# Performance work log

Hardware: AMD Instinct MI355X
Metric: run time of the kernel (lower is better)

The kernel has to match this reference:

```python
import jax, jax.numpy as jnp
import numpy as np

B, S, D = 2, 2048, 2048
H, KVH, HD = 16, 4, 128
ROT = 64  # partial rotary dims (cos/sin last dim = ROT//2)
WINDOW = 1024
EPS = 1e-6


def _rmsnorm(x, scale=None):
    x32 = x.astype(jnp.float32)
    y = x32 * jax.lax.rsqrt(jnp.mean(x32 * x32, axis=-1, keepdims=True) + EPS)
    if scale is not None:
        y = y * (1.0 + scale.astype(jnp.float32))
    return y.astype(x.dtype)


def _rope(x, cos, sin):
    # x: [b, h, s, hd]; rotate first ROT dims, pass through the rest
    x_rot, x_pass = x[..., :ROT], x[..., ROT:]
    x1, x2 = x_rot[..., :ROT // 2], x_rot[..., ROT // 2:]
    rotated = jnp.concatenate([-x2, x1], axis=-1)
    cos_f = jnp.concatenate([cos, cos], axis=-1)[None, None].astype(x.dtype)
    sin_f = jnp.concatenate([sin, sin], axis=-1)[None, None].astype(x.dtype)
    return jnp.concatenate([x_rot * cos_f + rotated * sin_f, x_pass], axis=-1)


def setup_inputs() -> dict:
    key = jax.random.key(0)
    ks = jax.random.split(key, 6)
    x = jax.random.normal(ks[0], (B, S, D), jnp.float32)
    # causal + sliding-window mask (True = masked out)
    i = jnp.arange(S)
    rel = i[:, None] - i[None, :]  # query - key
    mask = (rel < 0) | (rel >= WINDOW)
    # RoPE tables
    inv_freq = 1.0 / (10000.0 ** (jnp.arange(0, ROT, 2, dtype=jnp.float32) / ROT))
    t = jnp.arange(S, dtype=jnp.float32)[:, None] * inv_freq[None, :]  # [S, ROT//2]
    cos, sin = jnp.cos(t), jnp.sin(t)
    init = 0.02
    Wq = jax.random.normal(ks[1], (D, H * HD), jnp.float32) * init
    Wk = jax.random.normal(ks[2], (D, KVH * HD), jnp.float32) * init
    Wv = jax.random.normal(ks[3], (D, KVH * HD), jnp.float32) * init
    Wo = jax.random.normal(ks[4], (H * HD, D), jnp.float32) * init
    q_scale = jnp.zeros((HD,), jnp.float32)  # Gemma RMSNorm weight init = 0, applied as (1+w)
    k_scale = jnp.zeros((HD,), jnp.float32)
    return {"x": x, "mask": mask, "cos": cos, "sin": sin,
            "Wq": Wq, "Wk": Wk, "Wv": Wv, "Wo": Wo,
            "q_scale": q_scale, "k_scale": k_scale}


def reference(x, mask, cos, sin, Wq, Wk, Wv, Wo, q_scale, k_scale):
    b, s, _ = x.shape
    G = H // KVH  # group size
    q = (x @ Wq).reshape(b, s, H, HD).transpose(0, 2, 1, 3)      # [b,H,s,hd]
    q = _rope(_rmsnorm(q, q_scale), cos, sin)
    k = (x @ Wk).reshape(b, s, KVH, HD).transpose(0, 2, 1, 3)    # [b,KVH,s,hd]
    k = _rope(_rmsnorm(k, k_scale), cos, sin)
    v = _rmsnorm((x @ Wv).reshape(b, s, KVH, HD).transpose(0, 2, 1, 3))
    # grouped-head attention (equivalent to repeat_interleave of k/v over groups)
    qg = q.reshape(b, KVH, G, s, HD)
    scores = jnp.einsum('bkgqd,bkld->bkgql', qg, k)              # no 1/sqrt(hd): QK-norm model
    scores = jnp.where(mask[None, None, None], -jnp.inf, scores)
    w = jax.nn.softmax(scores.astype(jnp.float32), axis=-1).astype(q.dtype)
    ctx = jnp.einsum('bkgql,bkld->bkgqd', w, v)                  # [b,KVH,G,s,hd]
    ctx = ctx.reshape(b, H, s, HD).transpose(0, 2, 1, 3).reshape(b, s, H * HD)
    return ctx @ Wo
```

## Files before the change

### kernel.cpp

```cpp
#include <hip/hip_runtime.h>
#include <stdint.h>

#define B_ 2
#define S_ 2048
#define D_ 2048
#define H_ 16
#define KVH_ 4
#define HD_ 128
#define ROT_ 64
#define WINDOW_ 1024
#define EPS_ 1e-6f
#define M_ (B_ * S_)
#define NQKV_ 3072

#define QBLK 128
#define KVBLK 64
#define LOG2E 1.44269504088896340736f
#define DEFER_THR 8.0f

typedef unsigned short ushort_t;
typedef _Float16 f16;
typedef float f32x4 __attribute__((ext_vector_type(4)));
typedef f16 f16x8 __attribute__((ext_vector_type(8)));

#define NINF (-__builtin_inff())
#define EXP2F(x) __builtin_exp2f(x)

__device__ __forceinline__ void gload16(const void* g, void* l) {
  __builtin_amdgcn_global_load_lds(
      (const __attribute__((address_space(1))) void*)g,
      (__attribute__((address_space(3))) void*)l, 16, 0, 0);
}

__launch_bounds__(256, 4)
__global__ void cast_f32_f16(const float* __restrict__ src, f16* __restrict__ dst, int n8) {
  int i = blockIdx.x * 256 + threadIdx.x;
  if (i >= n8) return;
  float4 a = reinterpret_cast<const float4*>(src)[i * 2];
  float4 b = reinterpret_cast<const float4*>(src)[i * 2 + 1];
  f16x8 o = { (f16)a.x, (f16)a.y, (f16)a.z, (f16)a.w,
              (f16)b.x, (f16)b.y, (f16)b.z, (f16)b.w };
  reinterpret_cast<f16x8*>(dst)[i] = o;
}

__launch_bounds__(256, 4)
__global__ void transpose_f32_f16(const float* __restrict__ src, f16* __restrict__ dst,
                                  int R, int C) {
  __shared__ float tile[32][33];
  int c0 = blockIdx.x * 32, r0 = blockIdx.y * 32;
  int tx = threadIdx.x & 31, ty = threadIdx.x >> 5;
#pragma unroll
  for (int i = 0; i < 32; i += 8)
    tile[ty + i][tx] = src[(size_t)(r0 + ty + i) * C + c0 + tx];
  __syncthreads();
#pragma unroll
  for (int i = 0; i < 32; i += 8)
    dst[(size_t)(c0 + ty + i) * R + r0 + tx] = (f16)tile[tx][ty + i];
}

__launch_bounds__(256, 4)
__global__ void transpose16(const ushort_t* __restrict__ src, ushort_t* __restrict__ dst,
                            int R, int C) {
  __shared__ ushort_t tile[32][33];
  size_t base = (size_t)blockIdx.z * R * C;
  src += base; dst += base;
  int c0 = blockIdx.x * 32, r0 = blockIdx.y * 32;
  int tx = threadIdx.x & 31, ty = threadIdx.x >> 5;
#pragma unroll
  for (int i = 0; i < 32; i += 8)
    tile[ty + i][tx] = src[(size_t)(r0 + ty + i) * C + c0 + tx];
  __syncthreads();
#pragma unroll
  for (int i = 0; i < 32; i += 8)
    dst[(size_t)(c0 + ty + i) * R + r0 + tx] = tile[tx][ty + i];
}

__launch_bounds__(256, 2)
__global__ void gemm_f16(const f16* __restrict__ A, const f16* __restrict__ Bt,
                         float* __restrict__ C, int M, int N, int K) {
  __shared__ __attribute__((aligned(16))) f16 As[128][64];
  __shared__ __attribute__((aligned(16))) f16 Bs[128][64];
  const int gx = gridDim.x;
  const int nwg = gx * gridDim.y;
  const int flat = blockIdx.y * gx + blockIdx.x;
  const int q8 = nwg >> 3;
  const int id2 = (flat & 7) * q8 + (flat >> 3);
  const int bm = (id2 / gx) * 128, bn = (id2 % gx) * 128;
  const int tid = threadIdx.x;
  const int lane = tid & 63, wid = tid >> 6;
  const int wm = (wid >> 1) * 64, wn = (wid & 1) * 64;
  const int rr = lane & 15, rg = lane >> 4;
  const int sw = (((lane & 7) ^ (lane >> 3)) << 4);
  const int srw = lane >> 3;
  const char* Ab = (const char*)A + ((size_t)(bm + wid * 32 + srw) * K) * 2 + sw;
  const char* Bb = (const char*)Bt + ((size_t)(bn + wid * 32 + srw) * K) * 2 + sw;
  f32x4 acc[4][4] = {};
  for (int k0 = 0; k0 < K; k0 += 64) {
    __syncthreads();
#pragma unroll
    for (int g = 0; g < 4; ++g) {
      gload16(Ab + (size_t)(g * 8) * K * 2 + (size_t)k0 * 2,
              (char*)&As[0][0] + (wid * 32 + g * 8) * 128);
      gload16(Bb + (size_t)(g * 8) * K * 2 + (size_t)k0 * 2,
              (char*)&Bs[0][0] + (wid * 32 + g * 8) * 128);
    }
    __syncthreads();
    f16x8 af[4][2], bf[4][2];
#pragma unroll
    for (int i = 0; i < 4; ++i)
#pragma unroll
      for (int kk = 0; kk < 2; ++kk) {
        af[i][kk] = *reinterpret_cast<const f16x8*>(
            (const char*)&As[0][0] + (wm + i * 16 + rr) * 128 +
            ((kk * 64 + rg * 16) ^ ((rr & 7) << 4)));
        bf[i][kk] = *reinterpret_cast<const f16x8*>(
            (const char*)&Bs[0][0] + (wn + i * 16 + rr) * 128 +
            ((kk * 64 + rg * 16) ^ ((rr & 7) << 4)));
      }
#pragma unroll
    for (int kk = 0; kk < 2; ++kk)
#pragma unroll
      for (int i = 0; i < 4; ++i)
#pragma unroll
        for (int j = 0; j < 4; ++j)
          acc[i][j] = __builtin_amdgcn_mfma_f32_16x16x32_f16(af[i][kk], bf[j][kk],
                                                             acc[i][j], 0, 0, 0);
  }
#pragma unroll
  for (int i = 0; i < 4; ++i)
#pragma unroll
    for (int j = 0; j < 4; ++j)
#pragma unroll
      for (int r = 0; r < 4; ++r)
        C[(size_t)(bm + wm + i * 16 + rg * 4 + r) * N + (bn + wn + j * 16 + rr)] = acc[i][j][r];
}

__launch_bounds__(256, 4)
__global__ void norm_rope_kv(const float* __restrict__ qkv, const float* __restrict__ cosb,
                             const float* __restrict__ sinb, const float* __restrict__ ksc,
                             f16* __restrict__ kf, f16* __restrict__ vb) {
  int gw = blockIdx.x * 4 + (threadIdx.x >> 6);
  int lane = threadIdx.x & 63;
  int row = gw >> 3, c = gw & 7;
  int b = row >> 11, s = row & (S_ - 1);
  int col = (c < 4) ? (2048 + c * 128) : (2560 + (c - 4) * 128);
  const float* src = qkv + (size_t)row * NQKV_ + col;
  float2 v = *reinterpret_cast<const float2*>(src + lane * 2);
  float ss = v.x * v.x + v.y * v.y;
#pragma unroll
  for (int off = 32; off; off >>= 1) ss += __shfl_xor(ss, off);
  float inv = rsqrtf(ss * (1.0f / HD_) + EPS_);
  float x0 = v.x * inv, x1 = v.y * inv;
  int d0 = lane * 2;
  f16* dst;
  size_t idx;
  if (c < 4) {
    x0 *= (1.0f + ksc[d0]);
    x1 *= (1.0f + ksc[d0 + 1]);
    float y0 = __shfl_xor(x0, 16);
    float y1 = __shfl_xor(x1, 16);
    if (d0 < ROT_) {
      int dm = d0 & 31;
      float cs0 = cosb[s * 32 + dm],     sn0 = sinb[s * 32 + dm];
      float cs1 = cosb[s * 32 + dm + 1], sn1 = sinb[s * 32 + dm + 1];
      if (d0 < 32) { x0 = x0 * cs0 - y0 * sn0; x1 = x1 * cs1 - y1 * sn1; }
      else         { x0 = x0 * cs0 + y0 * sn0; x1 = x1 * cs1 + y1 * sn1; }
    }
    x0 *= LOG2E; x1 *= LOG2E;
    dst = kf; idx = ((size_t)((b * KVH_ + c) * S_ + s)) * HD_ + d0;
  } else {
    dst = vb; idx = ((size_t)((b * KVH_ + (c - 4)) * S_ + s)) * HD_ + d0;
  }
  f16 o[2] = { (f16)x0, (f16)x1 };
  unsigned int pk; __builtin_memcpy(&pk, o, 4);
  *reinterpret_cast<unsigned int*>(dst + idx) = pk;
}

__launch_bounds__(256, 2)
__global__ void flash_attn(const float* __restrict__ qkv, const float* __restrict__ cosb,
                           const float* __restrict__ sinb, const float* __restrict__ qsc,
                           const f16* __restrict__ kfp, const f16* __restrict__ vt,
                           f16* __restrict__ ctxf) {
  __shared__ __attribute__((aligned(16))) f16 Ks[2][KVBLK][128];
  __shared__ __attribute__((aligned(16))) f16 Vs[2][128][KVBLK];
  __shared__ __attribute__((aligned(16))) f16 Pb[4][32][40];
  const int id = blockIdx.x;
  const int g8 = id & 7, rest = id >> 3;
  const int b = g8 >> 2, kvh = g8 & 3;
  int hh, qtile;
  if (rest < 32) { hh = rest >> 3; qtile = 8 + (rest & 7); }
  else { int lv = rest - 32; hh = lv >> 3; qtile = lv & 7; }
  const int h = kvh * 4 + hh;
  const int lane = threadIdx.x & 63, w = threadIdx.x >> 6;
  const int rr = lane & 15, rg = lane >> 4;
  const int qBase = qtile * QBLK;
  const int qw = qBase + w * 32;
  const f16* Kh = kfp + (size_t)(b * KVH_ + kvh) * S_ * HD_;
  const f16* Vh = vt  + (size_t)(b * KVH_ + kvh) * HD_ * S_;

  f16x8 qf[2][4];
#pragma unroll
  for (int rb = 0; rb < 2; ++rb) {
    const int srow = qw + rb * 16 + rr;
    const float* qrow = qkv + (size_t)(b * S_ + srow) * NQKV_ + h * HD_;
    float qv[4][8];
    float ssq = 0.f;
#pragma unroll
    for (int kk = 0; kk < 4; ++kk) {
      float4 u0 = *reinterpret_cast<const float4*>(qrow + kk * 32 + rg * 8);
      float4 u1 = *reinterpret_cast<const float4*>(qrow + kk * 32 + rg * 8 + 4);
      qv[kk][0] = u0.x; qv[kk][1] = u0.y; qv[kk][2] = u0.z; qv[kk][3] = u0.w;
      qv[kk][4] = u1.x; qv[kk][5] = u1.y; qv[kk][6] = u1.z; qv[kk][7] = u1.w;
#pragma unroll
      for (int j = 0; j < 8; ++j) ssq += qv[kk][j] * qv[kk][j];
    }
    ssq += __shfl_xor(ssq, 16);
    ssq += __shfl_xor(ssq, 32);
    float inv = rsqrtf(ssq * (1.0f / HD_) + EPS_);
#pragma unroll
    for (int kk = 0; kk < 4; ++kk)
#pragma unroll
      for (int j = 0; j < 8; ++j)
        qv[kk][j] *= inv * (1.0f + qsc[kk * 32 + rg * 8 + j]);
    const float* cs = cosb + (size_t)srow * 32;
    const float* sn = sinb + (size_t)srow * 32;
#pragma unroll
    for (int j = 0; j < 8; ++j) {
      int d = rg * 8 + j;
      float c = cs[d], s = sn[d];
      float x0 = qv[0][j], x1 = qv[1][j];
      qv[0][j] = x0 * c - x1 * s;
      qv[1][j] = x1 * c + x0 * s;
    }
#pragma unroll
    for (int kk = 0; kk < 4; ++kk)
#pragma unroll
      for (int j = 0; j < 8; ++j)
        qf[rb][kk][j] = (f16)qv[kk][j];
  }

  f32x4 acc[2][8] = {};
  f32x4 accl[2] = {};
  float m_run[2][4], msafe[2][4];
#pragma unroll
  for (int rb = 0; rb < 2; ++rb)
#pragma unroll
    for (int r = 0; r < 4; ++r) { m_run[rb][r] = NINF; msafe[rb][r] = 0.f; }
  const f16x8 ones = { (f16)1, (f16)1, (f16)1, (f16)1, (f16)1, (f16)1, (f16)1, (f16)1 };

  int kvStart = qBase - (WINDOW_ - 1);
  if (kvStart < 0) kvStart = 0;
  kvStart &= ~(KVBLK - 1);
  const int ntile = (qBase + QBLK - kvStart) >> 6;

  const int k_r0 = lane >> 4;
  const int k_cb = (lane & 15) * 16;
  const int v_r0 = lane >> 3;
  const int v_cb = (lane & 7) * 16;

#define STAGE(bufs, key0_)                                                           \
  do {                                                                               \
    _Pragma("unroll")                                                                \
    for (int gg = 0; gg < 4; ++gg) {                                                 \
      int krow = gg * 4 + k_r0;                                                      \
      gload16((const char*)Kh + (size_t)((key0_) + w * 16 + krow) * 256 +            \
                  (k_cb ^ ((krow & 7) << 4)),                                        \
              (char*)&Ks[bufs][0][0] + (w * 16 + gg * 4) * 256);                     \
      int vrow = gg * 8 + v_r0;                                                      \
      gload16((const char*)Vh + (size_t)(w * 32 + vrow) * (S_ * 2) +                 \
                  (size_t)(key0_) * 2 + (v_cb ^ ((vrow & 7) << 4)),                  \
              (char*)&Vs[bufs][0][0] + (w * 32 + gg * 8) * 128);                     \
    }                                                                                \
  } while (0)

  STAGE(0, kvStart);
  __syncthreads();

  for (int t = 0; t < ntile; ++t) {
    const int key0 = kvStart + t * KVBLK;
    const int buf = t & 1;
    if (t + 1 < ntile) STAGE(buf ^ 1, key0 + KVBLK);

    const bool live = (key0 <= qw + 31) && (key0 + 63 >= qw - (WINDOW_ - 1));
    if (live) {
      f32x4 sc[2][4];
#pragma unroll
      for (int nt = 0; nt < 4; ++nt) {
        const int rt = nt * 16 + rr;
        const char* kbase = (const char*)&Ks[buf][0][0] + rt * 256;
        const int swz = (rt & 7) << 4;
        f16x8 kfr[4];
#pragma unroll
        for (int kk = 0; kk < 4; ++kk)
          kfr[kk] = *reinterpret_cast<const f16x8*>(kbase + ((kk * 64 + rg * 16) ^ swz));
        f32x4 s0 = {}, s1 = {};
#pragma unroll
        for (int kk = 0; kk < 4; ++kk) {
          s0 = __builtin_amdgcn_mfma_f32_16x16x32_f16(qf[0][kk], kfr[kk], s0, 0, 0, 0);
          s1 = __builtin_amdgcn_mfma_f32_16x16x32_f16(qf[1][kk], kfr[kk], s1, 0, 0, 0);
        }
        sc[0][nt] = s0; sc[1][nt] = s1;
      }

      const bool interior = (key0 + 63 <= qw) && (key0 >= qw - 992);
      if (!interior) {
#pragma unroll
        for (int rb = 0; rb < 2; ++rb)
#pragma unroll
          for (int nt = 0; nt < 4; ++nt)
#pragma unroll
            for (int r = 0; r < 4; ++r) {
              int qi = qw + rb * 16 + rg * 4 + r;
              int kj = key0 + nt * 16 + rr;
              bool valid = (kj <= qi) && (qi - kj < WINDOW_);
              if (!valid) sc[rb][nt][r] = NINF;
            }
      }

      float tmax[2][4];
#pragma unroll
      for (int rb = 0; rb < 2; ++rb)
#pragma unroll
        for (int r = 0; r < 4; ++r)
          tmax[rb][r] = fmaxf(fmaxf(sc[rb][0][r], sc[rb][1][r]),
                              fmaxf(sc[rb][2][r], sc[rb][3][r]));
#pragma unroll
      for (int off = 1; off < 16; off <<= 1)
#pragma unroll
        for (int rb = 0; rb < 2; ++rb)
#pragma unroll
          for (int r = 0; r < 4; ++r)
            tmax[rb][r] = fmaxf(tmax[rb][r], __shfl_xor(tmax[rb][r], off));

      bool defer = true;
#pragma unroll
      for (int rb = 0; rb < 2; ++rb)
#pragma unroll
        for (int r = 0; r < 4; ++r)
          defer = defer && (tmax[rb][r] - m_run[rb][r] <= DEFER_THR);
      if (!__all(defer)) {
#pragma unroll
        for (int rb = 0; rb < 2; ++rb) {
          float alpha[4];
#pragma unroll
          for (int r = 0; r < 4; ++r) {
            float mn = fmaxf(m_run[rb][r], tmax[rb][r]);
            alpha[r] = (m_run[rb][r] == NINF) ? 0.f : EXP2F(m_run[rb][r] - mn);
            m_run[rb][r] = mn;
            msafe[rb][r] = (mn == NINF) ? 0.f : mn;
          }
#pragma unroll
          for (int n = 0; n < 8; ++n)
#pragma unroll
            for (int r = 0; r < 4; ++r) acc[rb][n][r] *= alpha[r];
#pragma unroll
          for (int r = 0; r < 4; ++r) accl[rb][r] *= alpha[r];
        }
      }
#pragma unroll
      for (int rb = 0; rb < 2; ++rb)
#pragma unroll
        for (int nt = 0; nt < 4; ++nt)
#pragma unroll
          for (int r = 0; r < 4; ++r)
            sc[rb][nt][r] = EXP2F(sc[rb][nt][r] - msafe[rb][r]);

      f16x8 pf[2][2];
#pragma unroll
      for (int p = 0; p < 2; ++p) {
#pragma unroll
        for (int rb = 0; rb < 2; ++rb)
#pragma unroll
          for (int nt2 = 0; nt2 < 2; ++nt2)
#pragma unroll
            for (int r = 0; r < 4; ++r)
              Pb[w][rb * 16 + rg * 4 + r][nt2 * 16 + rr] = (f16)sc[rb][p * 2 + nt2][r];
        pf[0][p] = *reinterpret_cast<const f16x8*>(&Pb[w][rr][rg * 8]);
        pf[1][p] = *reinterpret_cast<const f16x8*>(&Pb[w][16 + rr][rg * 8]);
      }

      __builtin_amdgcn_s_setprio(1);
#pragma unroll
      for (int n = 0; n < 8; ++n) {
        const int d = n * 16 + rr;
        const char* vbase = (const char*)&Vs[buf][0][0] + d * 128;
        const int swz = (d & 7) << 4;
        f16x8 vf0 = *reinterpret_cast<const f16x8*>(vbase + ((rg * 16) ^ swz));
        f16x8 vf1 = *reinterpret_cast<const f16x8*>(vbase + ((64 + rg * 16) ^ swz));
        acc[0][n] = __builtin_amdgcn_mfma_f32_16x16x32_f16(pf[0][0], vf0, acc[0][n], 0, 0, 0);
        acc[0][n] = __builtin_amdgcn_mfma_f32_16x16x32_f16(pf[0][1], vf1, acc[0][n], 0, 0, 0);
        acc[1][n] = __builtin_amdgcn_mfma_f32_16x16x32_f16(pf[1][0], vf0, acc[1][n], 0, 0, 0);
        acc[1][n] = __builtin_amdgcn_mfma_f32_16x16x32_f16(pf[1][1], vf1, acc[1][n], 0, 0, 0);
      }
#pragma unroll
      for (int rb = 0; rb < 2; ++rb) {
        accl[rb] = __builtin_amdgcn_mfma_f32_16x16x32_f16(pf[rb][0], ones, accl[rb], 0, 0, 0);
        accl[rb] = __builtin_amdgcn_mfma_f32_16x16x32_f16(pf[rb][1], ones, accl[rb], 0, 0, 0);
      }
      __builtin_amdgcn_s_setprio(0);
    }

    __syncthreads();
  }
#undef STAGE

#pragma unroll
  for (int rb = 0; rb < 2; ++rb)
#pragma unroll
    for (int n = 0; n < 8; ++n)
#pragma unroll
      for (int r = 0; r < 4; ++r) {
        float o = acc[rb][n][r] / accl[rb][r];
        int qi = qw + rb * 16 + rg * 4 + r;
        ctxf[(size_t)(b * S_ + qi) * D_ + h * HD_ + n * 16 + rr] = (f16)o;
      }
}

extern "C" void kernel_launch(void* const* d_in, const int* in_sizes, int n_in,
                              void* d_out, int out_size, void* d_ws, size_t ws_size,
                              hipStream_t stream) {
  const float* x    = (const float*)d_in[0];
  const float* cosb = (const float*)d_in[2];
  const float* sinb = (const float*)d_in[3];
  const float* Wq   = (const float*)d_in[4];
  const float* Wk   = (const float*)d_in[5];
  const float* Wv   = (const float*)d_in[6];
  const float* Wo   = (const float*)d_in[7];
  const float* qsc  = (const float*)d_in[8];
  const float* ksc  = (const float*)d_in[9];
  float* out = (float*)d_out;

  char* ws = (char*)d_ws;
  const size_t MB = 1ull << 20;
  f16* xh    = (f16*)(ws + 0 * MB);
  f16* ctxf  = (f16*)(ws + 0 * MB);
  f16* wqkvT = (f16*)(ws + 16 * MB);
  f16* kf    = (f16*)(ws + 16 * MB);
  f16* vb    = (f16*)(ws + 20 * MB);
  f16* vtb   = (f16*)(ws + 24 * MB);
  f16* woT   = (f16*)(ws + 28 * MB);
  float* qkv = (float*)(ws + 36 * MB);

  cast_f32_f16<<<dim3(M_ * D_ / 8 / 256), 256, 0, stream>>>(x, xh, M_ * D_ / 8);
  transpose_f32_f16<<<dim3(64, 64), 256, 0, stream>>>(Wq, wqkvT, D_, 2048);
  transpose_f32_f16<<<dim3(16, 64), 256, 0, stream>>>(Wk, wqkvT + (size_t)2048 * D_, D_, 512);
  transpose_f32_f16<<<dim3(16, 64), 256, 0, stream>>>(Wv, wqkvT + (size_t)2560 * D_, D_, 512);
  transpose_f32_f16<<<dim3(64, 64), 256, 0, stream>>>(Wo, woT, D_, D_);
  gemm_f16<<<dim3(NQKV_ / 128, M_ / 128), 256, 0, stream>>>(xh, wqkvT, qkv, M_, NQKV_, D_);
  norm_rope_kv<<<dim3(M_ * 8 / 4), 256, 0, stream>>>(qkv, cosb, sinb, ksc, kf, vb);
  transpose16<<<dim3(HD_ / 32, S_ / 32, B_ * KVH_), 256, 0, stream>>>(
      (const ushort_t*)vb, (ushort_t*)vtb, S_, HD_);
  flash_attn<<<dim3((S_ / QBLK) * H_ * B_), 256, 0, stream>>>(
      qkv, cosb, sinb, qsc, kf, vtb, ctxf);
  gemm_f16<<<dim3(D_ / 128, M_ / 128), 256, 0, stream>>>(ctxf, woT, out, M_, D_, D_);
}
```

Before: 222.7 us.

## Switch attention to 32x32x16 MFMA with transposed S and register-only P handoff

```diff
diff --git a/kernel.cpp b/kernel.cpp
--- a/kernel.cpp
+++ b/kernel.cpp
@@ -21,6 +21,8 @@
 typedef unsigned short ushort_t;
 typedef _Float16 f16;
 typedef float f32x4 __attribute__((ext_vector_type(4)));
+typedef float f32x16 __attribute__((ext_vector_type(16)));
+typedef f16 f16x4 __attribute__((ext_vector_type(4)));
 typedef f16 f16x8 __attribute__((ext_vector_type(8)));
 
 #define NINF (-__builtin_inff())
@@ -30,6 +32,11 @@
   __builtin_amdgcn_global_load_lds(
       (const __attribute__((address_space(1))) void*)g,
       (__attribute__((address_space(3))) void*)l, 16, 0, 0);
+}
+
+__device__ __forceinline__ int cvtpk_i(float a, float b) {
+  auto h = __builtin_amdgcn_cvt_pkrtz(a, b);
+  int r; __builtin_memcpy(&r, &h, 4); return r;
 }
 
 __launch_bounds__(256, 4)
@@ -183,7 +190,6 @@
                            f16* __restrict__ ctxf) {
   __shared__ __attribute__((aligned(16))) f16 Ks[2][KVBLK][128];
   __shared__ __attribute__((aligned(16))) f16 Vs[2][128][KVBLK];
-  __shared__ __attribute__((aligned(16))) f16 Pb[4][32][40];
   const int id = blockIdx.x;
   const int g8 = id & 7, rest = id >> 3;
   const int b = g8 >> 2, kvh = g8 & 3;
@@ -192,61 +198,56 @@
   else { int lv = rest - 32; hh = lv >> 3; qtile = lv & 7; }
   const int h = kvh * 4 + hh;
   const int lane = threadIdx.x & 63, w = threadIdx.x >> 6;
-  const int rr = lane & 15, rg = lane >> 4;
+  const int ql = lane & 31;
+  const int hi = lane >> 5;
   const int qBase = qtile * QBLK;
   const int qw = qBase + w * 32;
+  const int q = qw + ql;
   const f16* Kh = kfp + (size_t)(b * KVH_ + kvh) * S_ * HD_;
   const f16* Vh = vt  + (size_t)(b * KVH_ + kvh) * HD_ * S_;
 
-  f16x8 qf[2][4];
-#pragma unroll
-  for (int rb = 0; rb < 2; ++rb) {
-    const int srow = qw + rb * 16 + rr;
-    const float* qrow = qkv + (size_t)(b * S_ + srow) * NQKV_ + h * HD_;
-    float qv[4][8];
+  f16x8 qf[8];
+  {
+    const float* qrow = qkv + (size_t)(b * S_ + q) * NQKV_ + h * HD_;
+    float qv[8][8];
     float ssq = 0.f;
 #pragma unroll
-    for (int kk = 0; kk < 4; ++kk) {
-      float4 u0 = *reinterpret_cast<const float4*>(qrow + kk * 32 + rg * 8);
-      float4 u1 = *reinterpret_cast<const float4*>(qrow + kk * 32 + rg * 8 + 4);
+    for (int kk = 0; kk < 8; ++kk) {
+      float4 u0 = *reinterpret_cast<const float4*>(qrow + kk * 16 + hi * 8);
+      float4 u1 = *reinterpret_cast<const float4*>(qrow + kk * 16 + hi * 8 + 4);
       qv[kk][0] = u0.x; qv[kk][1] = u0.y; qv[kk][2] = u0.z; qv[kk][3] = u0.w;
       qv[kk][4] = u1.x; qv[kk][5] = u1.y; qv[kk][6] = u1.z; qv[kk][7] = u1.w;
 #pragma unroll
       for (int j = 0; j < 8; ++j) ssq += qv[kk][j] * qv[kk][j];
     }
-    ssq += __shfl_xor(ssq, 16);
     ssq += __shfl_xor(ssq, 32);
     float inv = rsqrtf(ssq * (1.0f / HD_) + EPS_);
 #pragma unroll
-    for (int kk = 0; kk < 4; ++kk)
+    for (int kk = 0; kk < 8; ++kk)
 #pragma unroll
       for (int j = 0; j < 8; ++j)
-        qv[kk][j] *= inv * (1.0f + qsc[kk * 32 + rg * 8 + j]);
-    const float* cs = cosb + (size_t)srow * 32;
-    const float* sn = sinb + (size_t)srow * 32;
-#pragma unroll
-    for (int j = 0; j < 8; ++j) {
-      int d = rg * 8 + j;
-      float c = cs[d], s = sn[d];
-      float x0 = qv[0][j], x1 = qv[1][j];
-      qv[0][j] = x0 * c - x1 * s;
-      qv[1][j] = x1 * c + x0 * s;
-    }
-#pragma unroll
-    for (int kk = 0; kk < 4; ++kk)
+        qv[kk][j] *= inv * (1.0f + qsc[kk * 16 + hi * 8 + j]);
+    const float* cs = cosb + (size_t)q * 32;
+    const float* sn = sinb + (size_t)q * 32;
+#pragma unroll
+    for (int kk = 0; kk < 2; ++kk)
+#pragma unroll
+      for (int j = 0; j < 8; ++j) {
+        int d = kk * 16 + hi * 8 + j;
+        float c = cs[d], s_ = sn[d];
+        float x0 = qv[kk][j], x1 = qv[kk + 2][j];
+        qv[kk][j]     = x0 * c - x1 * s_;
+        qv[kk + 2][j] = x1 * c + x0 * s_;
+      }
+#pragma unroll
+    for (int kk = 0; kk < 8; ++kk)
 #pragma unroll
       for (int j = 0; j < 8; ++j)
-        qf[rb][kk][j] = (f16)qv[kk][j];
+        qf[kk][j] = (f16)qv[kk][j];
   }
 
-  f32x4 acc[2][8] = {};
-  f32x4 accl[2] = {};
-  float m_run[2][4], msafe[2][4];
-#pragma unroll
-  for (int rb = 0; rb < 2; ++rb)
-#pragma unroll
-    for (int r = 0; r < 4; ++r) { m_run[rb][r] = NINF; msafe[rb][r] = 0.f; }
-  const f16x8 ones = { (f16)1, (f16)1, (f16)1, (f16)1, (f16)1, (f16)1, (f16)1, (f16)1 };
+  f32x16 acc[4] = {};
+  float m_run = NINF, msafe = 0.f, l_run = 0.f;
 
   int kvStart = qBase - (WINDOW_ - 1);
   if (kvStart < 0) kvStart = 0;
@@ -283,119 +284,89 @@
 
     const bool live = (key0 <= qw + 31) && (key0 + 63 >= qw - (WINDOW_ - 1));
     if (live) {
-      f32x4 sc[2][4];
-#pragma unroll
-      for (int nt = 0; nt < 4; ++nt) {
-        const int rt = nt * 16 + rr;
+      f32x16 st[2];
+#pragma unroll
+      for (int kt = 0; kt < 2; ++kt) {
+        const int rt = kt * 32 + ql;
         const char* kbase = (const char*)&Ks[buf][0][0] + rt * 256;
         const int swz = (rt & 7) << 4;
-        f16x8 kfr[4];
-#pragma unroll
-        for (int kk = 0; kk < 4; ++kk)
-          kfr[kk] = *reinterpret_cast<const f16x8*>(kbase + ((kk * 64 + rg * 16) ^ swz));
-        f32x4 s0 = {}, s1 = {};
-#pragma unroll
-        for (int kk = 0; kk < 4; ++kk) {
-          s0 = __builtin_amdgcn_mfma_f32_16x16x32_f16(qf[0][kk], kfr[kk], s0, 0, 0, 0);
-          s1 = __builtin_amdgcn_mfma_f32_16x16x32_f16(qf[1][kk], kfr[kk], s1, 0, 0, 0);
+        f32x16 s = {};
+#pragma unroll
+        for (int kk = 0; kk < 8; ++kk) {
+          f16x8 kfr = *reinterpret_cast<const f16x8*>(kbase + ((kk * 32 + hi * 16) ^ swz));
+          s = __builtin_amdgcn_mfma_f32_32x32x16_f16(kfr, qf[kk], s, 0, 0, 0);
         }
-        sc[0][nt] = s0; sc[1][nt] = s1;
+        st[kt] = s;
       }
 
       const bool interior = (key0 + 63 <= qw) && (key0 >= qw - 992);
       if (!interior) {
 #pragma unroll
-        for (int rb = 0; rb < 2; ++rb)
-#pragma unroll
-          for (int nt = 0; nt < 4; ++nt)
-#pragma unroll
-            for (int r = 0; r < 4; ++r) {
-              int qi = qw + rb * 16 + rg * 4 + r;
-              int kj = key0 + nt * 16 + rr;
-              bool valid = (kj <= qi) && (qi - kj < WINDOW_);
-              if (!valid) sc[rb][nt][r] = NINF;
-            }
-      }
-
-      float tmax[2][4];
-#pragma unroll
-      for (int rb = 0; rb < 2; ++rb)
-#pragma unroll
-        for (int r = 0; r < 4; ++r)
-          tmax[rb][r] = fmaxf(fmaxf(sc[rb][0][r], sc[rb][1][r]),
-                              fmaxf(sc[rb][2][r], sc[rb][3][r]));
-#pragma unroll
-      for (int off = 1; off < 16; off <<= 1)
-#pragma unroll
-        for (int rb = 0; rb < 2; ++rb)
-#pragma unroll
-          for (int r = 0; r < 4; ++r)
-            tmax[rb][r] = fmaxf(tmax[rb][r], __shfl_xor(tmax[rb][r], off));
-
-      bool defer = true;
-#pragma unroll
-      for (int rb = 0; rb < 2; ++rb)
-#pragma unroll
-        for (int r = 0; r < 4; ++r)
-          defer = defer && (tmax[rb][r] - m_run[rb][r] <= DEFER_THR);
+        for (int kt = 0; kt < 2; ++kt)
+#pragma unroll
+          for (int r = 0; r < 16; ++r) {
+            int kj = key0 + kt * 32 + ((r & 3) + 8 * (r >> 2) + 4 * hi);
+            bool valid = (kj <= q) && (q - kj < WINDOW_);
+            if (!valid) st[kt][r] = NINF;
+          }
+      }
+
+      float tm = st[0][0];
+#pragma unroll
+      for (int r = 1; r < 16; ++r) tm = fmaxf(tm, st[0][r]);
+#pragma unroll
+      for (int r = 0; r < 16; ++r) tm = fmaxf(tm, st[1][r]);
+      tm = fmaxf(tm, __shfl_xor(tm, 32));
+
+      bool defer = (tm - m_run <= DEFER_THR);
       if (!__all(defer)) {
-#pragma unroll
-        for (int rb = 0; rb < 2; ++rb) {
-          float alpha[4];
-#pragma unroll
-          for (int r = 0; r < 4; ++r) {
-            float mn = fmaxf(m_run[rb][r], tmax[rb][r]);
-            alpha[r] = (m_run[rb][r] == NINF) ? 0.f : EXP2F(m_run[rb][r] - mn);
-            m_run[rb][r] = mn;
-            msafe[rb][r] = (mn == NINF) ? 0.f : mn;
-          }
-#pragma unroll
-          for (int n = 0; n < 8; ++n)
-#pragma unroll
-            for (int r = 0; r < 4; ++r) acc[rb][n][r] *= alpha[r];
-#pragma unroll
-          for (int r = 0; r < 4; ++r) accl[rb][r] *= alpha[r];
+        float mn = fmaxf(m_run, tm);
+        float alpha = (m_run == NINF) ? 0.f : EXP2F(m_run - mn);
+        m_run = mn;
+        msafe = (mn == NINF) ? 0.f : mn;
+#pragma unroll
+        for (int dt = 0; dt < 4; ++dt)
+#pragma unroll
+          for (int r = 0; r < 16; ++r) acc[dt][r] *= alpha;
+        l_run *= alpha;
+      }
+      float ps = 0.f;
+#pragma unroll
+      for (int kt = 0; kt < 2; ++kt)
+#pragma unroll
+        for (int r = 0; r < 16; ++r) {
+          float p = EXP2F(st[kt][r] - msafe);
+          st[kt][r] = p;
+          ps += p;
         }
-      }
-#pragma unroll
-      for (int rb = 0; rb < 2; ++rb)
-#pragma unroll
-        for (int nt = 0; nt < 4; ++nt)
-#pragma unroll
-          for (int r = 0; r < 4; ++r)
-            sc[rb][nt][r] = EXP2F(sc[rb][nt][r] - msafe[rb][r]);
-
-      f16x8 pf[2][2];
-#pragma unroll
-      for (int p = 0; p < 2; ++p) {
-#pragma unroll
-        for (int rb = 0; rb < 2; ++rb)
-#pragma unroll
-          for (int nt2 = 0; nt2 < 2; ++nt2)
-#pragma unroll
-            for (int r = 0; r < 4; ++r)
-              Pb[w][rb * 16 + rg * 4 + r][nt2 * 16 + rr] = (f16)sc[rb][p * 2 + nt2][r];
-        pf[0][p] = *reinterpret_cast<const f16x8*>(&Pb[w][rr][rg * 8]);
-        pf[1][p] = *reinterpret_cast<const f16x8*>(&Pb[w][16 + rr][rg * 8]);
+      ps += __shfl_xor(ps, 32);
+      l_run += ps;
+
+      f16x8 pf[4];
+#pragma unroll
+      for (int ks = 0; ks < 4; ++ks) {
+        const int kt = ks >> 1, rb = (ks & 1) * 8;
+        int w0 = cvtpk_i(st[kt][rb + 0], st[kt][rb + 1]);
+        int w2 = cvtpk_i(st[kt][rb + 4], st[kt][rb + 5]);
+        asm volatile("v_permlane32_swap_b32 %0, %1" : "+v"(w0), "+v"(w2));
+        int w1 = cvtpk_i(st[kt][rb + 2], st[kt][rb + 3]);
+        int w3 = cvtpk_i(st[kt][rb + 6], st[kt][rb + 7]);
+        asm volatile("v_permlane32_swap_b32 %0, %1" : "+v"(w1), "+v"(w3));
+        int wi[4] = { w0, w1, w2, w3 };
+        __builtin_memcpy(&pf[ks], wi, 16);
       }
 
       __builtin_amdgcn_s_setprio(1);
 #pragma unroll
-      for (int n = 0; n < 8; ++n) {
-        const int d = n * 16 + rr;
+      for (int dt = 0; dt < 4; ++dt) {
+        const int d = dt * 32 + ql;
         const char* vbase = (const char*)&Vs[buf][0][0] + d * 128;
         const int swz = (d & 7) << 4;
-        f16x8 vf0 = *reinterpret_cast<const f16x8*>(vbase + ((rg * 16) ^ swz));
-        f16x8 vf1 = *reinterpret_cast<const f16x8*>(vbase + ((64 + rg * 16) ^ swz));
-        acc[0][n] = __builtin_amdgcn_mfma_f32_16x16x32_f16(pf[0][0], vf0, acc[0][n], 0, 0, 0);
-        acc[0][n] = __builtin_amdgcn_mfma_f32_16x16x32_f16(pf[0][1], vf1, acc[0][n], 0, 0, 0);
-        acc[1][n] = __builtin_amdgcn_mfma_f32_16x16x32_f16(pf[1][0], vf0, acc[1][n], 0, 0, 0);
-        acc[1][n] = __builtin_amdgcn_mfma_f32_16x16x32_f16(pf[1][1], vf1, acc[1][n], 0, 0, 0);
-      }
-#pragma unroll
-      for (int rb = 0; rb < 2; ++rb) {
-        accl[rb] = __builtin_amdgcn_mfma_f32_16x16x32_f16(pf[rb][0], ones, accl[rb], 0, 0, 0);
-        accl[rb] = __builtin_amdgcn_mfma_f32_16x16x32_f16(pf[rb][1], ones, accl[rb], 0, 0, 0);
+#pragma unroll
+        for (int ks = 0; ks < 4; ++ks) {
+          f16x8 vf = *reinterpret_cast<const f16x8*>(vbase + ((ks * 32 + hi * 16) ^ swz));
+          acc[dt] = __builtin_amdgcn_mfma_f32_32x32x16_f16(vf, pf[ks], acc[dt], 0, 0, 0);
+        }
       }
       __builtin_amdgcn_s_setprio(0);
     }
@@ -404,16 +375,17 @@
   }
 #undef STAGE
 
-#pragma unroll
-  for (int rb = 0; rb < 2; ++rb)
-#pragma unroll
-    for (int n = 0; n < 8; ++n)
-#pragma unroll
-      for (int r = 0; r < 4; ++r) {
-        float o = acc[rb][n][r] / accl[rb][r];
-        int qi = qw + rb * 16 + rg * 4 + r;
-        ctxf[(size_t)(b * S_ + qi) * D_ + h * HD_ + n * 16 + rr] = (f16)o;
-      }
+  const float rinv = 1.0f / l_run;
+  f16* orow = ctxf + (size_t)(b * S_ + q) * D_ + h * HD_;
+#pragma unroll
+  for (int dt = 0; dt < 4; ++dt)
+#pragma unroll
+    for (int g = 0; g < 4; ++g) {
+      f16x4 o;
+#pragma unroll
+      for (int r = 0; r < 4; ++r) o[r] = (f16)(acc[dt][g * 4 + r] * rinv);
+      *reinterpret_cast<f16x4*>(orow + dt * 32 + 8 * g + 4 * hi) = o;
+    }
 }
 
 extern "C" void kernel_launch(void* const* d_in, const int* in_sizes, int n_in,
```

After: 206.4 us. 1.08x faster.
